# Optimization experiments

Measured on AMD Instinct MI355X. Metric: run time of the kernel, lower is better.

## Reference

```python
import jax, jax.numpy as jnp
import numpy as np

B, T, KQ, KT, NDOF = 1024, 1024, 15, 20, 7


def huber(x, delta=1.0):
    ax = jnp.abs(x)
    return jnp.where(ax < delta, 0.5 * x * x, delta * (ax - 0.5 * delta))


def setup_inputs() -> dict:
    key = jax.random.key(0)
    ks = jax.random.split(key, 12)
    q_cps = jax.random.normal(ks[0], (B, KQ, NDOF), dtype=jnp.float32)
    # time-spline control points must be positive so dtau_dt > 0
    t_cps = jax.random.uniform(ks[1], (B, KT, 1), dtype=jnp.float32) + 0.5
    # B-spline basis matrices for q(tau): [1, T, KQ]
    N = jax.random.normal(ks[2], (1, T, KQ), dtype=jnp.float32)
    dN = jax.random.normal(ks[3], (1, T, KQ), dtype=jnp.float32)
    ddN = jax.random.normal(ks[4], (1, T, KQ), dtype=jnp.float32)
    dddN = jax.random.normal(ks[5], (1, T, KQ), dtype=jnp.float32)
    # time-spline basis: Nt nonnegative so dtau_dt stays positive
    Nt = jax.random.uniform(ks[6], (1, T, KT), dtype=jnp.float32)
    dNt = jax.random.normal(ks[7], (1, T, KT), dtype=jnp.float32)
    ddNt = jax.random.normal(ks[8], (1, T, KT), dtype=jnp.float32)
    q_dot_limits = jnp.array([1.4835, 1.4835, 1.7453, 1.3090, 2.2689, 2.3562, 2.3562], dtype=jnp.float32)
    q_ddot_limits = 10.0 * q_dot_limits
    q_dddot_limits = 100.0 * q_dot_limits
    torque_limits = jnp.array([320.0, 320.0, 176.0, 176.0, 110.0, 40.0, 40.0], dtype=jnp.float32)
    return {"q_cps": q_cps, "t_cps": t_cps, "N": N, "dN": dN, "ddN": ddN,
            "dddN": dddN, "Nt": Nt, "dNt": dNt, "ddNt": ddNt,
            "q_dot_limits": q_dot_limits, "q_ddot_limits": q_ddot_limits,
            "q_dddot_limits": q_dddot_limits, "torque_limits": torque_limits}


def reference(q_cps, t_cps, N, dN, ddN, dddN, Nt, dNt, ddNt,
              q_dot_limits, q_ddot_limits, q_dddot_limits, torque_limits):
    # spline evaluations: [B, T, NDOF] and [B, T, 1]
    q = jnp.einsum('ijk,lkm->ljm', N, q_cps)
    q_dot_tau = jnp.einsum('ijk,lkm->ljm', dN, q_cps)
    q_ddot_tau = jnp.einsum('ijk,lkm->ljm', ddN, q_cps)
    q_dddot_tau = jnp.einsum('ijk,lkm->ljm', dddN, q_cps)
    dtau_dt = jnp.einsum('ijk,lkm->ljm', Nt, t_cps)
    ddtau_dtt = jnp.einsum('ijk,lkm->ljm', dNt, t_cps)
    dddtau_dttt = jnp.einsum('ijk,lkm->ljm', ddNt, t_cps)

    dt = 1.0 / dtau_dt[..., 0] / dtau_dt.shape[1]  # [B, T]
    t_cumsum = jnp.cumsum(dt, axis=-1)
    t = jnp.sum(dt, axis=-1)

    dtau_dt2 = dtau_dt ** 2
    q_dot = q_dot_tau * dtau_dt
    q_ddot = q_ddot_tau * dtau_dt2 + ddtau_dtt * q_dot_tau * dtau_dt
    q_dddot = (q_dddot_tau * dtau_dt ** 3
               + 3.0 * q_ddot_tau * ddtau_dtt * dtau_dt2
               + q_dot_tau * dtau_dt2 * dddtau_dttt
               + q_dot_tau * ddtau_dtt ** 2 * dtau_dt)

    # original rnea() returns zeros as the forward torque value
    torque = jnp.zeros_like(q)

    dt_e = dt[..., None]  # [B, T, 1]
    torque_loss = jnp.sum(huber(jax.nn.relu(jnp.abs(torque) - torque_limits)) * dt_e, axis=1)
    q_dot_loss = jnp.sum(huber(jax.nn.relu(jnp.abs(q_dot) - q_dot_limits)) * dt_e, axis=1)
    q_ddot_loss = jnp.sum(huber(jax.nn.relu(jnp.abs(q_ddot) - q_ddot_limits)) * dt_e, axis=1)
    q_dddot_loss = jnp.sum(huber(jax.nn.relu(jnp.abs(q_dddot) - q_dddot_limits)) * dt_e, axis=1)

    model_losses = jnp.concatenate([q_dot_loss, q_ddot_loss, q_dddot_loss], axis=-1)
    model_loss = jnp.sum(model_losses)
    return (model_loss, q_dot_loss, q_ddot_loss, q_dddot_loss, torque_loss,
            q, q_dot, q_ddot, q_dddot, torque, t, t_cumsum, dt)
```

## Files before the change

kernel.cpp:

```cpp
#include <hip/hip_runtime.h>

#define BB 1024
#define TT 1024
#define KQ 15
#define KT 20
#define NDOF 7

#define OFF_MODEL 0
#define OFF_QDL   1
#define OFF_QDDL  (1 + BB*NDOF)
#define OFF_QDDDL (1 + 2*BB*NDOF)
#define OFF_TQL   (1 + 3*BB*NDOF)
#define OFF_Q     (1 + 4*BB*NDOF)
#define OFF_QD    (OFF_Q    + (size_t)BB*TT*NDOF)
#define OFF_QDD   (OFF_QD   + (size_t)BB*TT*NDOF)
#define OFF_QDDD  (OFF_QDD  + (size_t)BB*TT*NDOF)
#define OFF_TQ    (OFF_QDDD + (size_t)BB*TT*NDOF)
#define OFF_T     (OFF_TQ   + (size_t)BB*TT*NDOF)
#define OFF_TCUM  (OFF_T    + (size_t)BB)
#define OFF_DT    (OFF_TCUM + (size_t)BB*TT)

__device__ __forceinline__ float hub(float v, float lim) {
    float x = fabsf(v) - lim;
    x = fmaxf(x, 0.0f);
    return (x < 1.0f) ? 0.5f * x * x : (x - 0.5f);
}

__device__ __forceinline__ void st4(float* p, float x0, float x1, float x2, float x3) {
    float v[4] = {x0, x1, x2, x3};
    __builtin_memcpy(p, v, 16);
}

__device__ __forceinline__ void st7(float* p, const float* a) {
    float v4[4] = {a[0], a[1], a[2], a[3]};
    __builtin_memcpy(p, v4, 16);
    float v2[2] = {a[4], a[5]};
    __builtin_memcpy(p + 4, v2, 8);
    p[6] = a[6];
}

__global__ __launch_bounds__(256, 4) void feas_fused(
    const float* __restrict__ q_cps, const float* __restrict__ t_cps,
    const float* __restrict__ Nb,  const float* __restrict__ dNb,
    const float* __restrict__ ddNb, const float* __restrict__ dddNb,
    const float* __restrict__ Ntb, const float* __restrict__ dNtb,
    const float* __restrict__ ddNtb,
    const float* __restrict__ qd_lim, const float* __restrict__ qdd_lim,
    const float* __restrict__ qddd_lim,
    float* __restrict__ out)
{
    const int b    = blockIdx.x;
    const int tid  = threadIdx.x;
    const int lane = tid & 63;
    const int w    = tid >> 6;

    __shared__ __align__(16) float sdt[TT];
    __shared__ float wsum[4];
    __shared__ float lossw[4][21];

    const float* cps = q_cps + (size_t)b * (KQ * NDOF);
    const float* tcp = t_cps + (size_t)b * KT;

    float tcr[KT];
    #pragma unroll
    for (int k = 0; k < KT; ++k) tcr[k] = tcp[k];

    float ls[21];
    #pragma unroll
    for (int j = 0; j < 21; ++j) ls[j] = 0.f;

    #pragma unroll 1
    for (int r = 0; r < TT / 256; ++r) {
        const int t = r * 256 + tid;

        const float* pt0 = Ntb   + (size_t)t * KT;
        const float* pt1 = dNtb  + (size_t)t * KT;
        const float* pt2 = ddNtb + (size_t)t * KT;
        float dtau = 0.f, ddtau = 0.f, dddtau = 0.f;
        #pragma unroll
        for (int k = 0; k < KT; ++k) {
            const float tc = tcr[k];
            dtau   = fmaf(pt0[k], tc, dtau);
            ddtau  = fmaf(pt1[k], tc, ddtau);
            dddtau = fmaf(pt2[k], tc, dddtau);
        }

        const float* p0 = Nb    + (size_t)t * KQ;
        const float* p1 = dNb   + (size_t)t * KQ;
        const float* p2 = ddNb  + (size_t)t * KQ;
        const float* p3 = dddNb + (size_t)t * KQ;
        float aq[NDOF], a1[NDOF], a2[NDOF], a3[NDOF];
        #pragma unroll
        for (int d = 0; d < NDOF; ++d) { aq[d] = 0.f; a1[d] = 0.f; a2[d] = 0.f; a3[d] = 0.f; }
        #pragma unroll
        for (int k = 0; k < KQ; ++k) {
            const float n0 = p0[k], n1 = p1[k], n2 = p2[k], n3 = p3[k];
            #pragma unroll
            for (int d = 0; d < NDOF; ++d) {
                const float cc = cps[k * NDOF + d];
                aq[d] = fmaf(n0, cc, aq[d]);
                a1[d] = fmaf(n1, cc, a1[d]);
                a2[d] = fmaf(n2, cc, a2[d]);
                a3[d] = fmaf(n3, cc, a3[d]);
            }
        }

        const float dtau2 = dtau * dtau;
        const float dtau3 = dtau2 * dtau;
        const float dtv   = 1.0f / (dtau * (float)TT);

        float qd[NDOF], qdd[NDOF], qddd[NDOF];
        #pragma unroll
        for (int d = 0; d < NDOF; ++d) {
            qd[d]   = a1[d] * dtau;
            qdd[d]  = a2[d] * dtau2 + ddtau * a1[d] * dtau;
            qddd[d] = a3[d] * dtau3 + 3.0f * a2[d] * ddtau * dtau2
                    + a1[d] * dtau2 * dddtau + a1[d] * ddtau * ddtau * dtau;
        }

        #pragma unroll
        for (int d = 0; d < NDOF; ++d) {
            ls[d]          += hub(qd[d],   qd_lim[d])   * dtv;
            ls[NDOF + d]   += hub(qdd[d],  qdd_lim[d])  * dtv;
            ls[2*NDOF + d] += hub(qddd[d], qddd_lim[d]) * dtv;
        }

        const size_t gb = (size_t)b * (TT * NDOF) + (size_t)t * NDOF;
        st7(out + OFF_Q    + gb, aq);
        st7(out + OFF_QD   + gb, qd);
        st7(out + OFF_QDD  + gb, qdd);
        st7(out + OFF_QDDD + gb, qddd);
        {
            float* z = out + OFF_TQ + gb;
            st4(z, 0.f, 0.f, 0.f, 0.f);
            float v2[2] = {0.f, 0.f};
            __builtin_memcpy(z + 4, v2, 8);
            z[6] = 0.f;
        }
        out[OFF_DT + (size_t)b * TT + t] = dtv;
        sdt[t] = dtv;
    }

    __syncthreads();

    const int s4 = 4 * tid;
    const float4 dvv = *(const float4*)(sdt + s4);
    const float c0 = dvv.x;
    const float c1 = c0 + dvv.y;
    const float c2 = c1 + dvv.z;
    const float c3 = c2 + dvv.w;
    float s = c3;
    #pragma unroll
    for (int off = 1; off < 64; off <<= 1) {
        const float u = __shfl_up(s, off);
        if (lane >= off) s += u;
    }
    if (lane == 63) wsum[w] = s;

    #pragma unroll
    for (int j = 0; j < 21; ++j) {
        float v = ls[j];
        #pragma unroll
        for (int off = 32; off > 0; off >>= 1) v += __shfl_down(v, off);
        ls[j] = v;
    }
    if (lane == 0) {
        #pragma unroll
        for (int j = 0; j < 21; ++j) lossw[w][j] = ls[j];
    }

    __syncthreads();

    float woff = 0.f;
    #pragma unroll
    for (int i = 0; i < 4; ++i) if (i < w) woff += wsum[i];
    const float excl = woff + (s - c3);
    st4(out + OFF_TCUM + (size_t)b * TT + s4,
        c0 + excl, c1 + excl, c2 + excl, c3 + excl);

    if (tid < 21) {
        const float acc = lossw[0][tid] + lossw[1][tid] + lossw[2][tid] + lossw[3][tid];
        const int which = tid / NDOF, d = tid - which * NDOF;
        const size_t o = (which == 0) ? (size_t)OFF_QDL
                       : (which == 1) ? (size_t)OFF_QDDL : (size_t)OFF_QDDDL;
        out[o + (size_t)b * NDOF + d] = acc;
    }
    if (tid < NDOF) out[OFF_TQL + (size_t)b * NDOF + tid] = 0.0f;
    if (tid == 0) {
        out[OFF_T + b] = wsum[0] + wsum[1] + wsum[2] + wsum[3];
        float p = 0.f;
        #pragma unroll
        for (int i = 0; i < 4; ++i) {
            #pragma unroll
            for (int j = 0; j < 21; ++j) p += lossw[i][j];
        }
        unsafeAtomicAdd(out + OFF_MODEL, p);
    }
}

extern "C" void kernel_launch(void* const* d_in, const int* in_sizes, int n_in,
                              void* d_out, int out_size, void* d_ws, size_t ws_size,
                              hipStream_t stream) {
    const float* q_cps    = (const float*)d_in[0];
    const float* t_cps    = (const float*)d_in[1];
    const float* Nb       = (const float*)d_in[2];
    const float* dNb      = (const float*)d_in[3];
    const float* ddNb     = (const float*)d_in[4];
    const float* dddNb    = (const float*)d_in[5];
    const float* Ntb      = (const float*)d_in[6];
    const float* dNtb     = (const float*)d_in[7];
    const float* ddNtb    = (const float*)d_in[8];
    const float* qd_lim   = (const float*)d_in[9];
    const float* qdd_lim  = (const float*)d_in[10];
    const float* qddd_lim = (const float*)d_in[11];
    float* out = (float*)d_out;

    hipMemsetAsync(out + OFF_MODEL, 0, sizeof(float), stream);

    feas_fused<<<dim3(BB), dim3(256), 0, stream>>>(
        q_cps, t_cps, Nb, dNb, ddNb, dddNb, Ntb, dNtb, ddNtb,
        qd_lim, qdd_lim, qddd_lim, out);
}
```

Baseline: 237.1 us.

## Split each batch row across two blocks with atomic loss merge

Each batch row is now handled by two blocks, each covering half of the time axis, which doubles the grid to 2048 blocks and raises the occupancy hint in launch bounds. The second-half block recomputes the dt values of the first half so it can offset its cumulative sum without any inter-block communication. Per-row losses are combined with atomics into outputs zeroed by a wider memset. This targets too few blocks per CU and the tail effect of 1024 large blocks, at the cost of redundant dtau work in the second half and extra atomics.

Result: slower. 319.7 us (+34.9%).

```diff
diff --git a/kernel.cpp b/kernel.cpp
--- a/kernel.cpp
+++ b/kernel.cpp
@@ -5,6 +5,7 @@
 #define KQ 15
 #define KT 20
 #define NDOF 7
+#define HT 512
 
 #define OFF_MODEL 0
 #define OFF_QDL   1
@@ -39,7 +40,12 @@
     p[6] = a[6];
 }
 
-__global__ __launch_bounds__(256, 4) void feas_fused(
+__device__ __forceinline__ void st2(float* p, float x0, float x1) {
+    float v[2] = {x0, x1};
+    __builtin_memcpy(p, v, 8);
+}
+
+__global__ __launch_bounds__(256, 8) void feas_fused(
     const float* __restrict__ q_cps, const float* __restrict__ t_cps,
     const float* __restrict__ Nb,  const float* __restrict__ dNb,
     const float* __restrict__ ddNb, const float* __restrict__ dddNb,
@@ -49,13 +55,16 @@
     const float* __restrict__ qddd_lim,
     float* __restrict__ out)
 {
-    const int b    = blockIdx.x;
+    const int bid  = blockIdx.x;
+    const int b    = bid >> 1;
+    const int h    = bid & 1;
     const int tid  = threadIdx.x;
     const int lane = tid & 63;
     const int w    = tid >> 6;
 
-    __shared__ __align__(16) float sdt[TT];
+    __shared__ __align__(16) float sdt[HT];
     __shared__ float wsum[4];
+    __shared__ float osw[4];
     __shared__ float lossw[4][21];
 
     const float* cps = q_cps + (size_t)b * (KQ * NDOF);
@@ -69,9 +78,12 @@
     #pragma unroll
     for (int j = 0; j < 21; ++j) ls[j] = 0.f;
 
+    const int t0 = h * HT;
+
     #pragma unroll 1
-    for (int r = 0; r < TT / 256; ++r) {
-        const int t = r * 256 + tid;
+    for (int r = 0; r < HT / 256; ++r) {
+        const int tl = r * 256 + tid;
+        const int t  = t0 + tl;
 
         const float* pt0 = Ntb   + (size_t)t * KT;
         const float* pt1 = dNtb  + (size_t)t * KT;
@@ -138,18 +150,31 @@
             z[6] = 0.f;
         }
         out[OFF_DT + (size_t)b * TT + t] = dtv;
-        sdt[t] = dtv;
-    }
-
+        sdt[tl] = dtv;
+    }
+
+    float osum = 0.f;
+    if (h) {
+        #pragma unroll 1
+        for (int r = 0; r < HT / 256; ++r) {
+            const int t = r * 256 + tid;
+            const float* pt0 = Ntb + (size_t)t * KT;
+            float dtau = 0.f;
+            #pragma unroll
+            for (int k = 0; k < KT; ++k) dtau = fmaf(pt0[k], tcr[k], dtau);
+            osum += 1.0f / (dtau * (float)TT);
+        }
+        #pragma unroll
+        for (int off = 32; off > 0; off >>= 1) osum += __shfl_down(osum, off);
+        if (lane == 0) osw[w] = osum;
+    }
     __syncthreads();
 
-    const int s4 = 4 * tid;
-    const float4 dvv = *(const float4*)(sdt + s4);
-    const float c0 = dvv.x;
-    const float c1 = c0 + dvv.y;
-    const float c2 = c1 + dvv.z;
-    const float c3 = c2 + dvv.w;
-    float s = c3;
+    const int e = 2 * tid;
+    const float2 dv = *(const float2*)(sdt + e);
+    const float c0 = dv.x;
+    const float c1 = c0 + dv.y;
+    float s = c1;
     #pragma unroll
     for (int off = 1; off < 64; off <<= 1) {
         const float u = __shfl_up(s, off);
@@ -171,23 +196,25 @@
 
     __syncthreads();
 
+    float base = 0.f;
+    if (h) base = osw[0] + osw[1] + osw[2] + osw[3];
     float woff = 0.f;
     #pragma unroll
     for (int i = 0; i < 4; ++i) if (i < w) woff += wsum[i];
-    const float excl = woff + (s - c3);
-    st4(out + OFF_TCUM + (size_t)b * TT + s4,
-        c0 + excl, c1 + excl, c2 + excl, c3 + excl);
+    const float pre = base + woff + (s - c1);
+    st2(out + OFF_TCUM + (size_t)b * TT + t0 + e, pre + c0, pre + c1);
+
+    if (h && tid == 0)
+        out[OFF_T + b] = base + wsum[0] + wsum[1] + wsum[2] + wsum[3];
 
     if (tid < 21) {
         const float acc = lossw[0][tid] + lossw[1][tid] + lossw[2][tid] + lossw[3][tid];
         const int which = tid / NDOF, d = tid - which * NDOF;
         const size_t o = (which == 0) ? (size_t)OFF_QDL
                        : (which == 1) ? (size_t)OFF_QDDL : (size_t)OFF_QDDDL;
-        out[o + (size_t)b * NDOF + d] = acc;
-    }
-    if (tid < NDOF) out[OFF_TQL + (size_t)b * NDOF + tid] = 0.0f;
+        unsafeAtomicAdd(out + o + (size_t)b * NDOF + d, acc);
+    }
     if (tid == 0) {
-        out[OFF_T + b] = wsum[0] + wsum[1] + wsum[2] + wsum[3];
         float p = 0.f;
         #pragma unroll
         for (int i = 0; i < 4; ++i) {
@@ -215,9 +242,9 @@
     const float* qddd_lim = (const float*)d_in[11];
     float* out = (float*)d_out;
 
-    hipMemsetAsync(out + OFF_MODEL, 0, sizeof(float), stream);
-
-    feas_fused<<<dim3(BB), dim3(256), 0, stream>>>(
+    hipMemsetAsync(out, 0, (size_t)(1 + 4 * BB * NDOF) * sizeof(float), stream);
+
+    feas_fused<<<dim3(2 * BB), dim3(256), 0, stream>>>(
         q_cps, t_cps, Nb, dNb, ddNb, dddNb, Ntb, dNtb, ddNtb,
         qd_lim, qdd_lim, qddd_lim, out);
 }
```
